# Kernel optimization log

Hardware: AMD Instinct MI355X
Metric: run time of the kernel (lower is better)

Reference implementation:

```python
import jax, jax.numpy as jnp
import numpy as np

VOCAB, D, H, B, S = 50257, 256, 512, 4096, 256
N_NODES, N_WORLDS = 10, 4
# static in-edge lists derived from SEFIROT_PATHS (to_sefirah == i)
IN_EDGES = [[], [0], [0, 1], [1], [2, 3], [2, 4], [1, 3, 5], [4, 5], [5, 6, 7], [6, 7, 8]]

def _gelu(v):
    return jax.nn.gelu(v, approximate=False)

def setup_inputs() -> dict:
    key = jax.random.key(0)
    ks = jax.random.split(key, 24)
    s = 0.02
    inp = {
        "x": jax.random.randint(ks[0], (B, S), 0, VOCAB, dtype=jnp.int64) if jax.config.jax_enable_x64 else jax.random.randint(ks[0], (B, S), 0, VOCAB, dtype=jnp.int32),
        "num_iterations": 3,
        "embed_table": jax.random.normal(ks[1], (VOCAB, D), jnp.float32) * s,
        # per-node processor MLP (stacked over 10 nodes), weights in [in,out] layout
        "node_w1": jax.random.normal(ks[2], (N_NODES, D, D), jnp.float32) * s,
        "node_b1": jnp.zeros((N_NODES, D), jnp.float32),
        "node_w2": jax.random.normal(ks[3], (N_NODES, D, D), jnp.float32) * s,
        "node_b2": jnp.zeros((N_NODES, D), jnp.float32),
        "recv_w": jax.random.normal(ks[4], (N_NODES, D, D), jnp.float32) * s,
        "recv_b": jnp.zeros((N_NODES, D), jnp.float32),
        # four worlds processors
        "world_w1": jax.random.normal(ks[5], (N_WORLDS, D, D), jnp.float32) * s,
        "world_b1": jnp.zeros((N_WORLDS, D), jnp.float32),
        "world_w2": jax.random.normal(ks[6], (N_WORLDS, D, D), jnp.float32) * s,
        "world_b2": jnp.zeros((N_WORLDS, D), jnp.float32),
        # tzimtzum
        "tz_w1": jax.random.normal(ks[7], (D, D // 2), jnp.float32) * s,
        "tz_b1": jnp.zeros((D // 2,), jnp.float32),
        "tz_w2": jax.random.normal(ks[8], (D // 2, D), jnp.float32) * s,
        "tz_b2": jnp.zeros((D,), jnp.float32),
        "void_space": jax.random.normal(ks[9], (D,), jnp.float32) * 0.1,
        "cre_w": jax.random.normal(ks[10], (D, D), jnp.float32) * s,
        "cre_b": jnp.zeros((D,), jnp.float32),
        # shekhinah head
        "shek_w1": jax.random.normal(ks[11], (D, H), jnp.float32) * s,
        "shek_b1": jnp.zeros((H,), jnp.float32),
        "shek_w2": jax.random.normal(ks[12], (H, 1), jnp.float32) * s,
        "shek_b2": jnp.zeros((1,), jnp.float32),
    }
    return inp

def _forward(embed_table, node_w1, node_b1, node_w2, node_b2, recv_w, recv_b,
             world_w1, world_b1, world_w2, world_b2,
             tz_w1, tz_b1, tz_w2, tz_b2, void_space, cre_w, cre_b,
             shek_w1, shek_b1, shek_w2, shek_b2, x, num_iterations):
    # memory-bound embedding gather [B,S,D] + mean over seq -> [B,D]
    embedded = jnp.take(embed_table, x, axis=0).mean(axis=1)
    states = [embedded] * N_NODES
    # sequential light-flow: node i within an iteration sees updated states of j < i
    for _ in range(int(num_iterations)):
        for i in range(N_NODES):
            h = _gelu(states[i] @ node_w1[i] + node_b1[i]) @ node_w2[i] + node_b2[i]
            srcs = IN_EDGES[i]
            if srcs:
                inc = states[srcs[0]]
                for s_ in srcs[1:]:
                    inc = inc + states[s_]
                h = h + inc @ recv_w[i] + recv_b[i]
            states[i] = h
    malkuth = states[9]
    cur = malkuth
    for w in range(N_WORLDS):
        cur = _gelu(cur @ world_w1[w] + world_b1[w]) @ world_w2[w] + world_b2[w]
    contracted = _gelu(cur @ tz_w1 + tz_b1) @ tz_w2 + tz_b2
    created = (contracted + void_space[None, :]) @ cre_w + cre_b
    shek = jax.nn.sigmoid(_gelu(created @ shek_w1 + shek_b1) @ shek_w2 + shek_b2)  # [B,1]
    # pack all outputs: [B, 10*D + D + D + 1]
    stacked = jnp.concatenate(states, axis=-1)
    return jnp.concatenate([stacked, cur, created, shek], axis=-1)

def reference(x, num_iterations, embed_table, node_w1, node_b1, node_w2, node_b2,
              recv_w, recv_b, world_w1, world_b1, world_w2, world_b2,
              tz_w1, tz_b1, tz_w2, tz_b2, void_space, cre_w, cre_b,
              shek_w1, shek_b1, shek_w2, shek_b2):
    return _forward(embed_table, node_w1, node_b1, node_w2, node_b2, recv_w, recv_b,
                    world_w1, world_b1, world_w2, world_b2,
                    tz_w1, tz_b1, tz_w2, tz_b2, void_space, cre_w, cre_b,
                    shek_w1, shek_b1, shek_w2, shek_b2, x, num_iterations)
```

## Files before the change

kernel.cpp:

```cpp
#include <hip/hip_runtime.h>
#include <hip/hip_bf16.h>

#define DIM 256
#define SEQ 256
#define NB 4096
#define OUT_STRIDE 3073

typedef float f32x4 __attribute__((ext_vector_type(4)));
typedef __bf16 bf16x8 __attribute__((ext_vector_type(8)));
typedef unsigned short u16;
typedef unsigned int u32;

__device__ __forceinline__ float bf2f(u16 h){ return __uint_as_float(((u32)h)<<16); }
__device__ __forceinline__ u16 f2bf(float f){
  u32 u = __float_as_uint(f);
  return (u16)((u + 0x7FFFu + ((u>>16)&1u)) >> 16);
}

__device__ const int d_nsrc[10] = {0,1,2,1,2,2,3,2,3,3};
__device__ const int d_srcs[10][3] = {{0,0,0},{0,0,0},{0,1,0},{1,0,0},{2,3,0},
                                      {2,4,0},{1,3,5},{4,5,0},{5,6,7},{6,7,8}};

__global__ void k_convert_table(const float* __restrict__ src, u16* __restrict__ dst, int n4){
  int i = blockIdx.x*blockDim.x + threadIdx.x;
  if (i >= n4) return;
  float4 v = ((const float4*)src)[i];
  ushort4 o; o.x=f2bf(v.x); o.y=f2bf(v.y); o.z=f2bf(v.z); o.w=f2bf(v.w);
  ((ushort4*)dst)[i] = o;
}

__global__ void k_pack(const float* __restrict__ nw1, const float* __restrict__ nw2,
                       const float* __restrict__ rw,  const float* __restrict__ ww1,
                       const float* __restrict__ ww2, const float* __restrict__ tw1,
                       const float* __restrict__ tw2, const float* __restrict__ cw,
                       const float* __restrict__ sw1, u16* __restrict__ dst){
  int g = blockIdx.x*blockDim.x + threadIdx.x;
  if (g >= 344064) return;
  const float* base; int gpm, K, N, segStart;
  if      (g < 81920) { base=nw1; gpm=8192; K=256; N=256; segStart=0; }
  else if (g < 163840){ base=nw2; gpm=8192; K=256; N=256; segStart=81920; }
  else if (g < 245760){ base=rw;  gpm=8192; K=256; N=256; segStart=163840; }
  else if (g < 278528){ base=ww1; gpm=8192; K=256; N=256; segStart=245760; }
  else if (g < 311296){ base=ww2; gpm=8192; K=256; N=256; segStart=278528; }
  else if (g < 315392){ base=tw1; gpm=4096; K=256; N=128; segStart=311296; }
  else if (g < 319488){ base=tw2; gpm=4096; K=128; N=256; segStart=315392; }
  else if (g < 327680){ base=cw;  gpm=8192; K=256; N=256; segStart=319488; }
  else                { base=sw1; gpm=16384;K=256; N=512; segStart=327680; }
  int gs = g - segStart;
  int mat = gs / gpm, gl = gs % gpm;
  int lane = gl & 63, g2 = gl >> 6;
  int Nt = N >> 4;
  int t = g2 % Nt, kk = g2 / Nt;
  int col = t*16 + (lane & 15);
  int k0  = kk*32 + (lane >> 4)*8;
  const float* m = base + (size_t)mat*K*N;
  u16* o = dst + (size_t)g*8;
  (void)K;
  #pragma unroll
  for (int j=0;j<8;j++) o[j] = f2bf(m[(size_t)(k0+j)*N + col]);
}

template<typename T>
__global__ void k_embed(const int* __restrict__ x, const T* __restrict__ table, u16* __restrict__ emb){
  __shared__ float red[4][256];
  int b = blockIdx.x;
  int tid = threadIdx.x, w = tid>>6, lane = tid&63;
  const int* xb = x + b*SEQ;
  float a0=0.f,a1=0.f,a2=0.f,a3=0.f;
  #pragma unroll 4
  for (int ii=0; ii<64; ii++){
    int idx = xb[w*64+ii];
    if constexpr (sizeof(T)==2){
      ushort4 v = *(const ushort4*)(table + (size_t)idx*DIM + lane*4);
      a0+=bf2f(v.x); a1+=bf2f(v.y); a2+=bf2f(v.z); a3+=bf2f(v.w);
    } else {
      float4 v = *(const float4*)(table + (size_t)idx*DIM + lane*4);
      a0+=v.x; a1+=v.y; a2+=v.z; a3+=v.w;
    }
  }
  red[w][lane*4+0]=a0; red[w][lane*4+1]=a1; red[w][lane*4+2]=a2; red[w][lane*4+3]=a3;
  __syncthreads();
  float s = (red[0][tid]+red[1][tid]+red[2][tid]+red[3][tid]) * (1.0f/SEQ);
  emb[(size_t)b*DIM + tid] = f2bf(s);
}

__device__ __forceinline__ bf16x8 lds_readA(const u16* base, int rs, int kk, int lane){
  int row = lane & 15;
  int kbyte = kk*64 + (lane>>4)*16;
  return *(const bf16x8*)((const char*)base + row*rs + (kbyte ^ ((row&7)<<4)));
}

template<int NPW, int NT, int KS>
__device__ __forceinline__ void gemm_pass(const u16* A, int rs, const bf16x8* __restrict__ wfb,
                                          f32x4* acc, int wave, int lane, int kk0 = 0){
  bf16x8 b[KS][NPW];
  #pragma unroll
  for (int kk=0; kk<KS; kk++)
    #pragma unroll
    for (int t=0; t<NPW; t++)
      b[kk][t] = wfb[((size_t)((kk0+kk)*NT + wave*NPW + t))*64 + lane];
  #pragma unroll
  for (int kk=0; kk<KS; kk++){
    bf16x8 a = lds_readA(A, rs, kk0+kk, lane);
    #pragma unroll
    for (int t=0; t<NPW; t++)
      acc[t] = __builtin_amdgcn_mfma_f32_16x16x32_bf16(a, b[kk][t], acc[t], 0, 0, 0);
  }
}

template<int NPW>
__device__ __forceinline__ void acc_init(f32x4* acc, const float* __restrict__ b1,
                                         const float* __restrict__ b2, int wave, int lane){
  #pragma unroll
  for (int t=0;t<NPW;t++){
    int col = (wave*NPW+t)*16 + (lane&15);
    float bv = b1 ? b1[col] : 0.0f;
    if (b2) bv += b2[col];
    f32x4 tmp = {bv,bv,bv,bv};
    acc[t] = tmp;
  }
}

template<int NPW, bool GELU>
__device__ __forceinline__ void epi_store(const f32x4* acc, u16* dst, int rs, int wave, int lane,
                                          const float* __restrict__ addcol){
  #pragma unroll
  for (int t=0;t<NPW;t++){
    int col = (wave*NPW+t)*16 + (lane&15);
    float add = addcol ? addcol[col] : 0.0f;
    #pragma unroll
    for (int r=0;r<4;r++){
      int row = (lane>>4)*4 + r;
      float v = acc[t][r];
      if (GELU) v = 0.5f*v*(1.0f + erff(v*0.70710678118654752f));
      v += add;
      *(u16*)((char*)dst + row*rs + ((col*2) ^ ((row&7)<<4))) = f2bf(v);
    }
  }
}

__device__ __forceinline__ void out_write(const u16* buf, int rs, float* __restrict__ out,
                                          size_t rowBase, int colBase, int wave, int lane){
  int r = wave;
  int sw = (r&7)<<4;
  #pragma unroll
  for (int cc=0; cc<4; cc++){
    int c = cc*64 + lane;
    float v = bf2f(*(const u16*)((const char*)buf + r*rs + ((c*2)^sw)));
    out[(rowBase + r)*OUT_STRIDE + colBase + c] = v;
  }
}

__global__ __launch_bounds__(1024,4) void k_main(
  const u16* __restrict__ wfrag, const u16* __restrict__ emb,
  const float* __restrict__ nb1, const float* __restrict__ nb2, const float* __restrict__ rb,
  const float* __restrict__ wb1, const float* __restrict__ wb2,
  const float* __restrict__ tb1, const float* __restrict__ tb2,
  const float* __restrict__ voidv, const float* __restrict__ cb,
  const float* __restrict__ sb1, const float* __restrict__ sb2, const float* __restrict__ sw2,
  const int* __restrict__ niter_p, float* __restrict__ out)
{
  __shared__ u16 states[10][16][256];
  __shared__ u16 abuf[16][512];
  __shared__ u16 cbuf[16][256];
  __shared__ u16 hbuf[16][512];
  __shared__ float red[16][65];

  const int tid = threadIdx.x, wave = tid>>6, lane = tid&63;
  const int blk = blockIdx.x;
  const int niter = *niter_p;
  const bf16x8* wf = (const bf16x8*)wfrag;

  {
    int r = tid >> 6, c0 = (tid & 63) * 4;
    uint2 v = *(const uint2*)(emb + ((size_t)(blk*16 + r))*DIM + c0);
    int sw = (r&7)<<4;
    #pragma unroll
    for (int st=0; st<10; st++){
      char* bp = (char*)states[st];
      *(uint2*)(bp + r*512 + ((c0*2) ^ sw)) = v;
    }
  }
  __syncthreads();

  for (int it=0; it<niter; it++){
    for (int i=0; i<10; i++){
      int ns = d_nsrc[i];
      f32x4 accA[1];
      acc_init<1>(accA, nb1 + i*DIM, nullptr, wave, lane);
      gemm_pass<1,16,8>(&states[i][0][0], 512, wf + (size_t)i*8192, accA, wave, lane);
      epi_store<1,true>(accA, &abuf[0][0], 1024, wave, lane, nullptr);
      if (ns > 0){
        int r = tid>>6, c0 = (tid&63)*4, sw = (r&7)<<4;
        const char* s0 = (const char*)states[d_srcs[i][0]];
        const char* s1 = (ns>1) ? (const char*)states[d_srcs[i][1]] : nullptr;
        const char* s2 = (ns>2) ? (const char*)states[d_srcs[i][2]] : nullptr;
        #pragma unroll
        for (int q=0;q<4;q++){
          int cbyte = ((c0+q)*2) ^ sw;
          float v = bf2f(*(const u16*)(s0 + r*512 + cbyte));
          if (s1) v += bf2f(*(const u16*)(s1 + r*512 + cbyte));
          if (s2) v += bf2f(*(const u16*)(s2 + r*512 + cbyte));
          *(u16*)((char*)abuf + r*1024 + 512 + cbyte) = f2bf(v);
        }
      }
      __syncthreads();
      f32x4 accB[1];
      acc_init<1>(accB, nb2 + i*DIM, (ns>0) ? (rb + i*DIM) : nullptr, wave, lane);
      gemm_pass<1,16,8>(&abuf[0][0], 1024, wf + 81920 + (size_t)i*8192, accB, wave, lane);
      if (ns > 0)
        gemm_pass<1,16,8>((const u16*)((const char*)&abuf[0][0] + 512), 1024,
                          wf + 163840 + (size_t)i*8192, accB, wave, lane);
      epi_store<1,false>(accB, &states[i][0][0], 512, wave, lane, nullptr);
      __syncthreads();
    }
  }

  for (int w=0; w<4; w++){
    f32x4 acc1[1];
    acc_init<1>(acc1, wb1 + w*DIM, nullptr, wave, lane);
    const u16* A = (w==0) ? &states[9][0][0] : &cbuf[0][0];
    gemm_pass<1,16,8>(A, 512, wf + 245760 + (size_t)w*8192, acc1, wave, lane);
    epi_store<1,true>(acc1, &abuf[0][0], 1024, wave, lane, nullptr);
    __syncthreads();
    f32x4 acc2[1];
    acc_init<1>(acc2, wb2 + w*DIM, nullptr, wave, lane);
    gemm_pass<1,16,8>(&abuf[0][0], 1024, wf + 278528 + (size_t)w*8192, acc2, wave, lane);
    epi_store<1,false>(acc2, &cbuf[0][0], 512, wave, lane, nullptr);
    __syncthreads();
  }
  out_write(&cbuf[0][0], 512, out, (size_t)blk*16, 2560, wave, lane);

  if (wave < 8){
    f32x4 acc[1];
    acc_init<1>(acc, tb1, nullptr, wave, lane);
    gemm_pass<1,8,8>(&cbuf[0][0], 512, wf + 311296, acc, wave, lane);
    epi_store<1,true>(acc, &abuf[0][0], 1024, wave, lane, nullptr);
  }
  __syncthreads();
  {
    f32x4 acc[1];
    acc_init<1>(acc, tb2, nullptr, wave, lane);
    gemm_pass<1,16,4>(&abuf[0][0], 1024, wf + 315392, acc, wave, lane);
    epi_store<1,false>(acc, &cbuf[0][0], 512, wave, lane, voidv);
    __syncthreads();
  }
  {
    f32x4 acc[1];
    acc_init<1>(acc, cb, nullptr, wave, lane);
    gemm_pass<1,16,8>(&cbuf[0][0], 512, wf + 319488, acc, wave, lane);
    epi_store<1,false>(acc, &abuf[0][0], 1024, wave, lane, nullptr);
    __syncthreads();
  }
  {
    f32x4 acc[2];
    acc_init<2>(acc, sb1, nullptr, wave, lane);
    gemm_pass<2,32,8>(&abuf[0][0], 1024, wf + 327680, acc, wave, lane);
    epi_store<2,true>(acc, &hbuf[0][0], 1024, wave, lane, nullptr);
    __syncthreads();
  }
  {
    int r = tid>>6, p = tid&63;
    int sw = (r&7)<<4;
    float partial = 0.f;
    #pragma unroll
    for (int j=0;j<8;j++){
      int k = p*8+j;
      partial += bf2f(*(const u16*)((const char*)hbuf + r*1024 + ((k*2)^sw))) * sw2[k];
    }
    red[r][p] = partial;
    __syncthreads();
    if (tid < 16){
      float s = sb2[0];
      #pragma unroll
      for (int p2=0;p2<64;p2++) s += red[tid][p2];
      out[((size_t)(blk*16+tid))*OUT_STRIDE + 3072] = 1.f/(1.f+expf(-s));
    }
  }

  #pragma unroll
  for (int st=0; st<10; st++)
    out_write(&states[st][0][0], 512, out, (size_t)blk*16, st*256, wave, lane);
  out_write(&abuf[0][0], 1024, out, (size_t)blk*16, 2816, wave, lane);
}

extern "C" void kernel_launch(void* const* d_in, const int* in_sizes, int n_in,
                              void* d_out, int out_size, void* d_ws, size_t ws_size,
                              hipStream_t stream){
  const int*   x     = (const int*)d_in[0];
  const int*   nitp  = (const int*)d_in[1];
  const float* table = (const float*)d_in[2];
  const float* nw1   = (const float*)d_in[3];
  const float* nb1   = (const float*)d_in[4];
  const float* nw2   = (const float*)d_in[5];
  const float* nb2   = (const float*)d_in[6];
  const float* rw    = (const float*)d_in[7];
  const float* rb    = (const float*)d_in[8];
  const float* ww1   = (const float*)d_in[9];
  const float* wb1   = (const float*)d_in[10];
  const float* ww2   = (const float*)d_in[11];
  const float* wb2   = (const float*)d_in[12];
  const float* tw1   = (const float*)d_in[13];
  const float* tb1   = (const float*)d_in[14];
  const float* tw2   = (const float*)d_in[15];
  const float* tb2   = (const float*)d_in[16];
  const float* voidv = (const float*)d_in[17];
  const float* cw    = (const float*)d_in[18];
  const float* cb    = (const float*)d_in[19];
  const float* sw1   = (const float*)d_in[20];
  const float* sb1   = (const float*)d_in[21];
  const float* sw2   = (const float*)d_in[22];
  const float* sb2   = (const float*)d_in[23];
  float* out = (float*)d_out;
  char* ws = (char*)d_ws;

  const size_t TBL_BYTES = (size_t)50257*256*2;
  const size_t WF_BYTES  = (size_t)344064*8*2;
  const size_t EMB_BYTES = (size_t)4096*256*2;
  bool big = ws_size >= TBL_BYTES + WF_BYTES + EMB_BYTES;

  u16 *tbl16, *wfrag, *emb;
  if (big){ tbl16=(u16*)ws; wfrag=(u16*)(ws+TBL_BYTES); emb=(u16*)(ws+TBL_BYTES+WF_BYTES); }
  else    { tbl16=nullptr;  wfrag=(u16*)ws;             emb=(u16*)(ws+WF_BYTES); }

  k_pack<<<1344, 256, 0, stream>>>(nw1,nw2,rw,ww1,ww2,tw1,tw2,cw,sw1,wfrag);
  if (big){
    k_convert_table<<<(3216448+255)/256, 256, 0, stream>>>(table, tbl16, 3216448);
    k_embed<u16><<<NB, 256, 0, stream>>>(x, tbl16, emb);
  } else {
    k_embed<float><<<NB, 256, 0, stream>>>(x, table, emb);
  }
  k_main<<<256, 1024, 0, stream>>>(wfrag, emb, nb1, nb2, rb, wb1, wb2, tb1, tb2,
                                   voidv, cb, sb1, sb2, sw2, nitp, out);
}
```

Baseline: 292.2 us.

## Software-pipeline weight fragment loads across GEMM stages and use tanh GELU

Adds a double-buffered register pipeline so each stage's weight fragments and bias values are prefetched from global memory while the previous stage's MFMAs run. This hides load latency across the serial chain of small GEMMs. It also replaces the erf GELU with the tanh approximation using __expf, vectorises the in-edge sum, and writes the state outputs during the last iteration instead of at the end. The tanh GELU departs from the exact erf reference, and the doubled fragment registers raise register pressure at 1024 threads per block.

```diff
diff --git a/kernel.cpp b/kernel.cpp
--- a/kernel.cpp
+++ b/kernel.cpp
@@ -15,6 +15,12 @@
 __device__ __forceinline__ u16 f2bf(float f){
   u32 u = __float_as_uint(f);
   return (u16)((u + 0x7FFFu + ((u>>16)&1u)) >> 16);
+}
+__device__ __forceinline__ float gelu_f(float x){
+  float u = 0.7978845608028654f*(x + 0.044715f*x*x*x);
+  float e = __expf(2.0f*u);
+  float t = 1.0f - 2.0f/(e+1.0f);
+  return 0.5f*x*(1.0f+t);
 }
 
 __device__ const int d_nsrc[10] = {0,1,2,1,2,2,3,2,3,3};
@@ -90,52 +96,43 @@
   return *(const bf16x8*)((const char*)base + row*rs + (kbyte ^ ((row&7)<<4)));
 }
 
-template<int NPW, int NT, int KS>
-__device__ __forceinline__ void gemm_pass(const u16* A, int rs, const bf16x8* __restrict__ wfb,
-                                          f32x4* acc, int wave, int lane, int kk0 = 0){
-  bf16x8 b[KS][NPW];
-  #pragma unroll
-  for (int kk=0; kk<KS; kk++)
-    #pragma unroll
-    for (int t=0; t<NPW; t++)
-      b[kk][t] = wfb[((size_t)((kk0+kk)*NT + wave*NPW + t))*64 + lane];
-  #pragma unroll
-  for (int kk=0; kk<KS; kk++){
-    bf16x8 a = lds_readA(A, rs, kk0+kk, lane);
-    #pragma unroll
-    for (int t=0; t<NPW; t++)
-      acc[t] = __builtin_amdgcn_mfma_f32_16x16x32_bf16(a, b[kk][t], acc[t], 0, 0, 0);
-  }
-}
-
-template<int NPW>
-__device__ __forceinline__ void acc_init(f32x4* acc, const float* __restrict__ b1,
-                                         const float* __restrict__ b2, int wave, int lane){
-  #pragma unroll
-  for (int t=0;t<NPW;t++){
-    int col = (wave*NPW+t)*16 + (lane&15);
-    float bv = b1 ? b1[col] : 0.0f;
-    if (b2) bv += b2[col];
-    f32x4 tmp = {bv,bv,bv,bv};
-    acc[t] = tmp;
-  }
-}
-
-template<int NPW, bool GELU>
-__device__ __forceinline__ void epi_store(const f32x4* acc, u16* dst, int rs, int wave, int lane,
-                                          const float* __restrict__ addcol){
-  #pragma unroll
-  for (int t=0;t<NPW;t++){
-    int col = (wave*NPW+t)*16 + (lane&15);
-    float add = addcol ? addcol[col] : 0.0f;
-    #pragma unroll
-    for (int r=0;r<4;r++){
-      int row = (lane>>4)*4 + r;
-      float v = acc[t][r];
-      if (GELU) v = 0.5f*v*(1.0f + erff(v*0.70710678118654752f));
-      v += add;
-      *(u16*)((char*)dst + row*rs + ((col*2) ^ ((row&7)<<4))) = f2bf(v);
-    }
+template<int KS>
+__device__ __forceinline__ void loadB(bf16x8* dst, const bf16x8* __restrict__ w,
+                                      int idx0, int nt, int lane){
+  #pragma unroll
+  for (int kk=0;kk<KS;kk++) dst[kk] = w[((size_t)(kk*nt+idx0))*64 + lane];
+}
+template<int KS>
+__device__ __forceinline__ void copyB(bf16x8* d, const bf16x8* s){
+  #pragma unroll
+  for (int kk=0;kk<KS;kk++) d[kk]=s[kk];
+}
+template<int KS>
+__device__ __forceinline__ void mfmaK(const u16* A, int rs, const bf16x8* b, f32x4& acc, int lane){
+  #pragma unroll
+  for (int kk=0;kk<KS;kk++){
+    bf16x8 a = lds_readA(A, rs, kk, lane);
+    acc = __builtin_amdgcn_mfma_f32_16x16x32_bf16(a, b[kk], acc, 0, 0, 0);
+  }
+}
+
+__device__ __forceinline__ f32x4 acc_make(float bv){
+  f32x4 t = {bv,bv,bv,bv};
+  return t;
+}
+
+template<bool GELU>
+__device__ __forceinline__ void epi1(f32x4 acc, u16* dst, int rs, int colbase, int lane,
+                                     const float* __restrict__ addcol){
+  int col = colbase + (lane&15);
+  float add = addcol ? addcol[col] : 0.0f;
+  #pragma unroll
+  for (int r=0;r<4;r++){
+    int row = (lane>>4)*4 + r;
+    float v = acc[r];
+    if (GELU) v = gelu_f(v);
+    v += add;
+    *(u16*)((char*)dst + row*rs + ((col*2) ^ ((row&7)<<4))) = f2bf(v);
   }
 }
 
@@ -170,6 +167,7 @@
   const int blk = blockIdx.x;
   const int niter = *niter_p;
   const bf16x8* wf = (const bf16x8*)wfrag;
+  const int bcol = wave*16 + (lane&15);
 
   {
     int r = tid >> 6, c0 = (tid & 63) * 4;
@@ -183,82 +181,137 @@
   }
   __syncthreads();
 
+  bf16x8 bcur[8], bnext[8];
+  float bn1, bn2;
+  loadB<8>(bcur, (niter>0) ? wf : (wf + 245760), wave, 16, lane);
+  bn1 = (niter>0) ? nb1[bcol] : wb1[bcol];
+  bn2 = 0.f;
+
   for (int it=0; it<niter; it++){
+    bool last = (it == niter-1);
     for (int i=0; i<10; i++){
       int ns = d_nsrc[i];
-      f32x4 accA[1];
-      acc_init<1>(accA, nb1 + i*DIM, nullptr, wave, lane);
-      gemm_pass<1,16,8>(&states[i][0][0], 512, wf + (size_t)i*8192, accA, wave, lane);
-      epi_store<1,true>(accA, &abuf[0][0], 1024, wave, lane, nullptr);
+      float c1 = bn1;
+      loadB<8>(bnext, wf + 81920 + (size_t)i*8192, wave, 16, lane);
+      bn1 = nb2[i*DIM + bcol];
+      bn2 = (ns>0) ? rb[i*DIM + bcol] : 0.f;
+      f32x4 accA = acc_make(c1);
+      mfmaK<8>(&states[i][0][0], 512, bcur, accA, lane);
+      epi1<true>(accA, &abuf[0][0], 1024, wave*16, lane, nullptr);
       if (ns > 0){
-        int r = tid>>6, c0 = (tid&63)*4, sw = (r&7)<<4;
-        const char* s0 = (const char*)states[d_srcs[i][0]];
-        const char* s1 = (ns>1) ? (const char*)states[d_srcs[i][1]] : nullptr;
-        const char* s2 = (ns>2) ? (const char*)states[d_srcs[i][2]] : nullptr;
-        #pragma unroll
-        for (int q=0;q<4;q++){
-          int cbyte = ((c0+q)*2) ^ sw;
-          float v = bf2f(*(const u16*)(s0 + r*512 + cbyte));
-          if (s1) v += bf2f(*(const u16*)(s1 + r*512 + cbyte));
-          if (s2) v += bf2f(*(const u16*)(s2 + r*512 + cbyte));
-          *(u16*)((char*)abuf + r*1024 + 512 + cbyte) = f2bf(v);
-        }
+        int r = wave, sw = (r&7)<<4;
+        int off = ((lane*8) ^ sw);
+        const char* s0 = (const char*)states[d_srcs[i][0]] + r*512;
+        const char* s1 = (ns>1) ? ((const char*)states[d_srcs[i][1]] + r*512) : nullptr;
+        const char* s2 = (ns>2) ? ((const char*)states[d_srcs[i][2]] + r*512) : nullptr;
+        uint2 v0 = *(const uint2*)(s0+off);
+        uint2 v1, v2; v1.x=v1.y=0u; v2.x=v2.y=0u;
+        if (s1) v1 = *(const uint2*)(s1+off);
+        if (s2) v2 = *(const uint2*)(s2+off);
+        float ax = __uint_as_float(v0.x<<16) + __uint_as_float(v1.x<<16) + __uint_as_float(v2.x<<16);
+        float bx = __uint_as_float(v0.x&0xffff0000u) + __uint_as_float(v1.x&0xffff0000u) + __uint_as_float(v2.x&0xffff0000u);
+        float ay = __uint_as_float(v0.y<<16) + __uint_as_float(v1.y<<16) + __uint_as_float(v2.y<<16);
+        float by = __uint_as_float(v0.y&0xffff0000u) + __uint_as_float(v1.y&0xffff0000u) + __uint_as_float(v2.y&0xffff0000u);
+        uint2 o; o.x = (u32)f2bf(ax) | ((u32)f2bf(bx)<<16);
+        o.y = (u32)f2bf(ay) | ((u32)f2bf(by)<<16);
+        *(uint2*)((char*)abuf + r*1024 + 512 + off) = o;
       }
       __syncthreads();
-      f32x4 accB[1];
-      acc_init<1>(accB, nb2 + i*DIM, (ns>0) ? (rb + i*DIM) : nullptr, wave, lane);
-      gemm_pass<1,16,8>(&abuf[0][0], 1024, wf + 81920 + (size_t)i*8192, accB, wave, lane);
-      if (ns > 0)
-        gemm_pass<1,16,8>((const u16*)((const char*)&abuf[0][0] + 512), 1024,
-                          wf + 163840 + (size_t)i*8192, accB, wave, lane);
-      epi_store<1,false>(accB, &states[i][0][0], 512, wave, lane, nullptr);
+      copyB<8>(bcur, bnext);
+      float d1 = bn1, d2 = bn2;
+      const bf16x8* nextAw = (i<9) ? (wf + (size_t)(i+1)*8192)
+                                   : (!last ? wf : (wf + 245760));
+      f32x4 accB = acc_make(d1 + d2);
+      if (ns > 0){
+        loadB<8>(bnext, wf + 163840 + (size_t)i*8192, wave, 16, lane);
+        mfmaK<8>(&abuf[0][0], 1024, bcur, accB, lane);
+        copyB<8>(bcur, bnext);
+        loadB<8>(bnext, nextAw, wave, 16, lane);
+        bn1 = (i<9) ? nb1[(i+1)*DIM + bcol] : (!last ? nb1[bcol] : wb1[bcol]);
+        bn2 = 0.f;
+        mfmaK<8>((const u16*)((const char*)&abuf[0][0] + 512), 1024, bcur, accB, lane);
+      } else {
+        loadB<8>(bnext, nextAw, wave, 16, lane);
+        bn1 = (i<9) ? nb1[(i+1)*DIM + bcol] : (!last ? nb1[bcol] : wb1[bcol]);
+        bn2 = 0.f;
+        mfmaK<8>(&abuf[0][0], 1024, bcur, accB, lane);
+      }
+      epi1<false>(accB, &states[i][0][0], 512, wave*16, lane, nullptr);
       __syncthreads();
+      copyB<8>(bcur, bnext);
+      if (last)
+        out_write(&states[i][0][0], 512, out, (size_t)blk*16, i*256, wave, lane);
     }
   }
 
   for (int w=0; w<4; w++){
-    f32x4 acc1[1];
-    acc_init<1>(acc1, wb1 + w*DIM, nullptr, wave, lane);
-    const u16* A = (w==0) ? &states[9][0][0] : &cbuf[0][0];
-    gemm_pass<1,16,8>(A, 512, wf + 245760 + (size_t)w*8192, acc1, wave, lane);
-    epi_store<1,true>(acc1, &abuf[0][0], 1024, wave, lane, nullptr);
+    float c1 = bn1;
+    loadB<8>(bnext, wf + 278528 + (size_t)w*8192, wave, 16, lane);
+    bn1 = wb2[w*DIM + bcol];
+    f32x4 a1 = acc_make(c1);
+    mfmaK<8>((w==0) ? &states[9][0][0] : &cbuf[0][0], 512, bcur, a1, lane);
+    epi1<true>(a1, &abuf[0][0], 1024, wave*16, lane, nullptr);
     __syncthreads();
-    f32x4 acc2[1];
-    acc_init<1>(acc2, wb2 + w*DIM, nullptr, wave, lane);
-    gemm_pass<1,16,8>(&abuf[0][0], 1024, wf + 278528 + (size_t)w*8192, acc2, wave, lane);
-    epi_store<1,false>(acc2, &cbuf[0][0], 512, wave, lane, nullptr);
+    copyB<8>(bcur, bnext);
+    float d1 = bn1;
+    if (w < 3){
+      loadB<8>(bnext, wf + 245760 + (size_t)(w+1)*8192, wave, 16, lane);
+      bn1 = wb1[(w+1)*DIM + bcol];
+    } else {
+      loadB<8>(bnext, wf + 311296, wave, 8, lane);
+      bn1 = tb1[bcol & 127];
+    }
+    f32x4 a2 = acc_make(d1);
+    mfmaK<8>(&abuf[0][0], 1024, bcur, a2, lane);
+    epi1<false>(a2, &cbuf[0][0], 512, wave*16, lane, nullptr);
     __syncthreads();
+    copyB<8>(bcur, bnext);
   }
   out_write(&cbuf[0][0], 512, out, (size_t)blk*16, 2560, wave, lane);
 
-  if (wave < 8){
-    f32x4 acc[1];
-    acc_init<1>(acc, tb1, nullptr, wave, lane);
-    gemm_pass<1,8,8>(&cbuf[0][0], 512, wf + 311296, acc, wave, lane);
-    epi_store<1,true>(acc, &abuf[0][0], 1024, wave, lane, nullptr);
-  }
-  __syncthreads();
-  {
-    f32x4 acc[1];
-    acc_init<1>(acc, tb2, nullptr, wave, lane);
-    gemm_pass<1,16,4>(&abuf[0][0], 1024, wf + 315392, acc, wave, lane);
-    epi_store<1,false>(acc, &cbuf[0][0], 512, wave, lane, voidv);
-    __syncthreads();
-  }
-  {
-    f32x4 acc[1];
-    acc_init<1>(acc, cb, nullptr, wave, lane);
-    gemm_pass<1,16,8>(&cbuf[0][0], 512, wf + 319488, acc, wave, lane);
-    epi_store<1,false>(acc, &abuf[0][0], 1024, wave, lane, nullptr);
-    __syncthreads();
-  }
-  {
-    f32x4 acc[2];
-    acc_init<2>(acc, sb1, nullptr, wave, lane);
-    gemm_pass<2,32,8>(&abuf[0][0], 1024, wf + 327680, acc, wave, lane);
-    epi_store<2,true>(acc, &hbuf[0][0], 1024, wave, lane, nullptr);
-    __syncthreads();
-  }
+  bf16x8 b4[4];
+  loadB<4>(b4, wf + 315392, wave, 16, lane);
+  {
+    float c1 = bn1;
+    bn1 = tb2[bcol];
+    if (wave < 8){
+      f32x4 a = acc_make(c1);
+      mfmaK<8>(&cbuf[0][0], 512, bcur, a, lane);
+      epi1<true>(a, &abuf[0][0], 1024, wave*16, lane, nullptr);
+    }
+  }
+  __syncthreads();
+  loadB<8>(bnext, wf + 319488, wave, 16, lane);
+  {
+    float c1 = bn1;
+    bn1 = cb[bcol];
+    f32x4 a = acc_make(c1);
+    mfmaK<4>(&abuf[0][0], 1024, b4, a, lane);
+    epi1<false>(a, &cbuf[0][0], 512, wave*16, lane, voidv);
+  }
+  __syncthreads();
+  copyB<8>(bcur, bnext);
+  loadB<8>(bnext, wf + 327680, wave*2, 32, lane);
+  {
+    float c1 = bn1;
+    bn1 = sb1[wave*32 + (lane&15)];
+    bn2 = sb1[wave*32 + 16 + (lane&15)];
+    f32x4 a = acc_make(c1);
+    mfmaK<8>(&cbuf[0][0], 512, bcur, a, lane);
+    epi1<false>(a, &abuf[0][0], 1024, wave*16, lane, nullptr);
+  }
+  __syncthreads();
+  copyB<8>(bcur, bnext);
+  loadB<8>(bnext, wf + 327680, wave*2+1, 32, lane);
+  {
+    f32x4 a0 = acc_make(bn1);
+    f32x4 a1 = acc_make(bn2);
+    mfmaK<8>(&abuf[0][0], 1024, bcur, a0, lane);
+    mfmaK<8>(&abuf[0][0], 1024, bnext, a1, lane);
+    epi1<true>(a0, &hbuf[0][0], 1024, (wave*2+0)*16, lane, nullptr);
+    epi1<true>(a1, &hbuf[0][0], 1024, (wave*2+1)*16, lane, nullptr);
+  }
+  __syncthreads();
   {
     int r = tid>>6, p = tid&63;
     int sw = (r&7)<<4;
@@ -274,13 +327,9 @@
       float s = sb2[0];
       #pragma unroll
       for (int p2=0;p2<64;p2++) s += red[tid][p2];
-      out[((size_t)(blk*16+tid))*OUT_STRIDE + 3072] = 1.f/(1.f+expf(-s));
-    }
-  }
-
-  #pragma unroll
-  for (int st=0; st<10; st++)
-    out_write(&states[st][0][0], 512, out, (size_t)blk*16, st*256, wave, lane);
+      out[((size_t)(blk*16+tid))*OUT_STRIDE + 3072] = 1.f/(1.f+__expf(-s));
+    }
+  }
   out_write(&abuf[0][0], 1024, out, (size_t)blk*16, 2816, wave, lane);
 }
 
```

New measurement: 343.5 us. 1.18x slower.
